# Kernel optimization log

Hardware: AMD Instinct MI355X
Metric: run time of the kernel (lower is better)

The kernel has to match this reference:

```python
import jax, jax.numpy as jnp
import numpy as np

B = 2048      # batch
C = 200       # n_country
F = 32        # n_feat_country == n_input
H = 256       # n_hidden


def setup_inputs() -> dict:
    key = jax.random.key(0)
    ks = jax.random.split(key, 9)
    x = jax.random.normal(ks[0], (B, C * F), dtype=jnp.float32)
    transition = jax.random.uniform(ks[1], (C, C), dtype=jnp.float32) / C
    W1 = jax.random.normal(ks[2], (F, H), dtype=jnp.float32) * (1.0 / np.sqrt(F))
    b1 = jax.random.normal(ks[3], (H,), dtype=jnp.float32) * 0.01
    W2 = jax.random.normal(ks[4], (H, H), dtype=jnp.float32) * (1.0 / np.sqrt(H))
    b2 = jax.random.normal(ks[5], (H,), dtype=jnp.float32) * 0.01
    W3 = jax.random.normal(ks[6], (H, 1), dtype=jnp.float32) * (1.0 / np.sqrt(H))
    b3 = jax.random.normal(ks[7], (1,), dtype=jnp.float32) * 0.01
    return {"x": x, "transition": transition, "W1": W1, "b1": b1,
            "W2": W2, "b2": b2, "W3": W3, "b3": b3}


def reference(x, transition, W1, b1, W2, b2, W3, b3):
    Bsz, N = x.shape
    Cn = transition.shape[0]
    Ff = N // Cn
    xc = x.reshape(Bsz, Cn, Ff)            # per-country feature blocks
    S = xc[..., 0]                          # [B, C] susceptible (feature 0)
    I = xc[..., 1]                          # [B, C] infected   (feature 1)
    # transition-weighted neighbor aggregation (the python loop == one GEMM)
    sinflow = S @ transition                # [B, C]
    iinflow = I @ transition                # [B, C]
    outflow = 1.0 - jnp.diag(transition)    # [C]
    # shared tiny MLP applied per country (vectorized over C)
    h = jax.nn.relu(jnp.einsum('bcf,fh->bch', xc, W1) + b1)
    h = jax.nn.relu(jnp.einsum('bch,hk->bck', h, W2) + b2)
    lamb = (jnp.einsum('bch,ho->bco', h, W3) + b3)[..., 0]  # [B, C]
    dS = -lamb * S + sinflow - outflow * S
    dI = lamb * S + iinflow - outflow * I
    # interleave: pred[:, 2i] = S_i + dS_i, pred[:, 2i+1] = I_i + dI_i
    pred = jnp.stack([S + dS, I + dI], axis=-1).reshape(Bsz, 2 * Cn)
    return pred
```

## Files before the change

kernel.cpp:

```cpp
#include <hip/hip_runtime.h>
#include <stdint.h>

#define M_ROWS 409600
#define B_CNT  2048
#define C_CNT  200
#define N_TILES (M_ROWS / 64)
#define GRID_MLP 512

typedef __attribute__((ext_vector_type(8))) short bf16x8;
typedef __attribute__((ext_vector_type(4))) float f32x4;

__device__ __forceinline__ ushort f2bf(float f) {
    uint32_t u = __float_as_uint(f);
    u += 0x7fffu + ((u >> 16) & 1u);
    return (ushort)(u >> 16);
}

__device__ __forceinline__ uint32_t cvtpk_bf16(float lo, float hi) {
    uint32_t r;
    asm("v_cvt_pk_bf16_f32 %0, %1, %2" : "=v"(r) : "v"(lo), "v"(hi));
    return r;
}

__device__ __forceinline__ f32x4 mfma16(bf16x8 a, bf16x8 b, f32x4 c) {
    return __builtin_amdgcn_mfma_f32_16x16x32_bf16(a, b, c, 0, 0, 0);
}

__device__ __forceinline__ bf16x8 pack8(float4 a, float4 b) {
    bf16x8 r;
    r[0] = (short)f2bf(a.x); r[1] = (short)f2bf(a.y);
    r[2] = (short)f2bf(a.z); r[3] = (short)f2bf(a.w);
    r[4] = (short)f2bf(b.x); r[5] = (short)f2bf(b.y);
    r[6] = (short)f2bf(b.z); r[7] = (short)f2bf(b.w);
    return r;
}

__global__ __launch_bounds__(256) void prep_kernel(
    const float* __restrict__ x, const float* __restrict__ T,
    const float* __restrict__ W1, const float* __restrict__ W2,
    ushort* __restrict__ xb16, float* __restrict__ Sc, float* __restrict__ Ic,
    float* __restrict__ sinW, float* __restrict__ iinW,
    ushort* __restrict__ W1t, ushort* __restrict__ W2t, int do_xb) {
    int blk = blockIdx.x, t = threadIdx.x;
    if (blk < B_CNT) {
        __shared__ float Sr[C_CNT], Ir[C_CNT];
        const float4* xr = (const float4*)(x + (size_t)blk * 6400);
        ushort4* xw = (ushort4*)(xb16 + (size_t)blk * 6400);
#pragma unroll
        for (int i = 0; i < 7; ++i) {
            int i4 = i * 256 + t;
            if (i4 < 1600) {
                float4 v = xr[i4];
                if (do_xb) {
                    ushort4 u;
                    u.x = f2bf(v.x); u.y = f2bf(v.y);
                    u.z = f2bf(v.z); u.w = f2bf(v.w);
                    xw[i4] = u;
                }
                if ((i4 & 7) == 0) {
                    int c = i4 >> 3;
                    Sr[c] = v.x; Ir[c] = v.y;
                    Sc[blk * C_CNT + c] = v.x;
                    Ic[blk * C_CNT + c] = v.y;
                }
            }
        }
        __syncthreads();
        if (t < C_CNT) {
            float as = 0.f, ai = 0.f;
            for (int cp = 0; cp < C_CNT; ++cp) {
                float tv = T[cp * C_CNT + t];
                as = fmaf(Sr[cp], tv, as);
                ai = fmaf(Ir[cp], tv, ai);
            }
            sinW[blk * C_CNT + t] = as;
            iinW[blk * C_CNT + t] = ai;
        }
    } else if (blk < B_CNT + 256) {
        int n = blk - B_CNT;
        W2t[n * 256 + t] = f2bf(W2[t * 256 + n]);
    } else {
        int idx = (blk - B_CNT - 256) * 256 + t;
        int n = idx >> 5, k = idx & 31;
        W1t[idx] = f2bf(W1[k * 256 + n]);
    }
}

template <bool XB>
__global__ __launch_bounds__(256, 2) void mlp_kernel(
    const float* __restrict__ x,
    const ushort* __restrict__ xb16,
    const float* __restrict__ T,
    const float* __restrict__ b1,
    const float* __restrict__ b2,
    const float* __restrict__ W3,
    const float* __restrict__ b3,
    const ushort* __restrict__ W1t,
    const ushort* __restrict__ W2t,
    const float* __restrict__ Sc, const float* __restrict__ Ic,
    const float* __restrict__ sinW, const float* __restrict__ iinW,
    float* __restrict__ out) {
    constexpr int RS = 264;
    __shared__ ushort h1s[64 * RS];
    __shared__ float b1f[256], b2f[256], w3f[256];
    __shared__ float lamb2[2][4][64];

    const int tid  = threadIdx.x;
    const int w    = tid >> 6;
    const int lane = tid & 63;
    const int L    = lane & 15;
    const int q    = lane >> 4;

    b1f[tid] = b1[tid];
    b2f[tid] = b2[tid];
    w3f[tid] = W3[tid];
    const float b3v = b3[0];

    bf16x8 a2r[4][8];
#pragma unroll
    for (int i2 = 0; i2 < 4; ++i2)
#pragma unroll
        for (int kc = 0; kc < 8; ++kc)
            a2r[i2][kc] =
                *(const bf16x8*)(W2t + (64 * w + i2 * 16 + L) * 256 + kc * 32 + q * 8);

    bf16x8 aw[4];
#pragma unroll
    for (int i = 0; i < 4; ++i)
        aw[i] = *(const bf16x8*)(W1t + (64 * w + i * 16 + L) * 32 + q * 8);

    int tile = blockIdx.x;
    bf16x8 bx[4];
#pragma unroll
    for (int i = 0; i < 4; ++i) {
        if (XB) {
            bx[i] = *(const bf16x8*)(xb16 + (size_t)(tile * 64 + i * 16 + L) * 32 + q * 8);
        } else {
            const float4* xr =
                (const float4*)(x + (size_t)(tile * 64 + i * 16 + L) * 32 + q * 8);
            bx[i] = pack8(xr[0], xr[1]);
        }
    }

    float eS = 0.f, eI = 0.f, esv = 0.f, eiv = 0.f, eof = 0.f;
    int ptile = -1;
    int p = 0;

    for (; tile < N_TILES; tile += GRID_MLP) {
        f32x4 acc1[4][4];
#pragma unroll
        for (int i1 = 0; i1 < 4; ++i1)
#pragma unroll
            for (int im = 0; im < 4; ++im)
                acc1[i1][im] = mfma16(aw[i1], bx[im], (f32x4){0.f, 0.f, 0.f, 0.f});

        {
            int tn = tile + GRID_MLP;
            if (tn >= N_TILES) tn = tile;
            const size_t mn0 = (size_t)tn * 64;
#pragma unroll
            for (int i = 0; i < 4; ++i) {
                if (XB) {
                    bx[i] = *(const bf16x8*)(xb16 + (mn0 + i * 16 + L) * 32 + q * 8);
                } else {
                    const float4* xr =
                        (const float4*)(x + (mn0 + i * 16 + L) * 32 + q * 8);
                    bx[i] = pack8(xr[0], xr[1]);
                }
            }
        }

        __syncthreads();

#pragma unroll
        for (int i1 = 0; i1 < 4; ++i1) {
            int n1b = 64 * w + i1 * 16 + q * 4;
            const float4 bv = *reinterpret_cast<const float4*>(&b1f[n1b]);
#pragma unroll
            for (int im = 0; im < 4; ++im) {
                int m = im * 16 + L;
                float v0 = fmaxf(acc1[i1][im][0] + bv.x, 0.f);
                float v1 = fmaxf(acc1[i1][im][1] + bv.y, 0.f);
                float v2 = fmaxf(acc1[i1][im][2] + bv.z, 0.f);
                float v3 = fmaxf(acc1[i1][im][3] + bv.w, 0.f);
                uint2 pk;
                pk.x = cvtpk_bf16(v0, v1);
                pk.y = cvtpk_bf16(v2, v3);
                *reinterpret_cast<uint2*>(&h1s[m * RS + n1b]) = pk;
            }
        }

        if (ptile >= 0 && tid < 64) {
            int gm = ptile * 64 + tid;
            float lam = lamb2[p ^ 1][0][tid] + lamb2[p ^ 1][1][tid] +
                        lamb2[p ^ 1][2][tid] + lamb2[p ^ 1][3][tid] + b3v;
            float dS = -lam * eS + esv - eof * eS;
            float dI =  lam * eS + eiv - eof * eI;
            float2 o; o.x = eS + dS; o.y = eI + dI;
            ((float2*)out)[gm] = o;
        }

        __syncthreads();

        f32x4 acc2[4][4];
#pragma unroll
        for (int i2 = 0; i2 < 4; ++i2)
#pragma unroll
            for (int im = 0; im < 4; ++im) acc2[i2][im] = (f32x4){0.f, 0.f, 0.f, 0.f};

#pragma unroll
        for (int kc = 0; kc < 8; ++kc) {
            bf16x8 bh[4];
#pragma unroll
            for (int im = 0; im < 4; ++im) {
                int m = im * 16 + L;
                bh[im] = *(const bf16x8*)(&h1s[m * RS + kc * 32 + q * 8]);
            }
#pragma unroll
            for (int i2 = 0; i2 < 4; ++i2)
#pragma unroll
                for (int im = 0; im < 4; ++im)
                    acc2[i2][im] = mfma16(a2r[i2][kc], bh[im], acc2[i2][im]);
        }

        if (tid < 64) {
            int gm = tile * 64 + tid;
            eS  = Sc[gm];  eI  = Ic[gm];
            esv = sinW[gm]; eiv = iinW[gm];
            int c = gm % C_CNT;
            eof = 1.0f - T[c * C_CNT + c];
        }

        float part[4] = {0.f, 0.f, 0.f, 0.f};
#pragma unroll
        for (int i2 = 0; i2 < 4; ++i2) {
            int n2b = 64 * w + i2 * 16 + q * 4;
            const float4 b2v = *reinterpret_cast<const float4*>(&b2f[n2b]);
            const float4 w3v = *reinterpret_cast<const float4*>(&w3f[n2b]);
#pragma unroll
            for (int im = 0; im < 4; ++im) {
                float h0 = fmaxf(acc2[i2][im][0] + b2v.x, 0.f);
                float h1 = fmaxf(acc2[i2][im][1] + b2v.y, 0.f);
                float h2 = fmaxf(acc2[i2][im][2] + b2v.z, 0.f);
                float h3 = fmaxf(acc2[i2][im][3] + b2v.w, 0.f);
                part[im] = fmaf(h0, w3v.x, part[im]);
                part[im] = fmaf(h1, w3v.y, part[im]);
                part[im] = fmaf(h2, w3v.z, part[im]);
                part[im] = fmaf(h3, w3v.w, part[im]);
            }
        }
#pragma unroll
        for (int im = 0; im < 4; ++im) {
            float pp = part[im];
            pp += __shfl_xor(pp, 16);
            pp += __shfl_xor(pp, 32);
            if (q == 0) lamb2[p][w][im * 16 + L] = pp;
        }

        ptile = tile;
        p ^= 1;
    }

    __syncthreads();
    if (ptile >= 0 && tid < 64) {
        int gm = ptile * 64 + tid;
        float lam = lamb2[p ^ 1][0][tid] + lamb2[p ^ 1][1][tid] +
                    lamb2[p ^ 1][2][tid] + lamb2[p ^ 1][3][tid] + b3v;
        float dS = -lam * eS + esv - eof * eS;
        float dI =  lam * eS + eiv - eof * eI;
        float2 o; o.x = eS + dS; o.y = eI + dI;
        ((float2*)out)[gm] = o;
    }
}

extern "C" void kernel_launch(void* const* d_in, const int* in_sizes, int n_in,
                              void* d_out, int out_size, void* d_ws, size_t ws_size,
                              hipStream_t stream) {
    const float* x  = (const float*)d_in[0];
    const float* T  = (const float*)d_in[1];
    const float* W1 = (const float*)d_in[2];
    const float* b1 = (const float*)d_in[3];
    const float* W2 = (const float*)d_in[4];
    const float* b2 = (const float*)d_in[5];
    const float* W3 = (const float*)d_in[6];
    const float* b3 = (const float*)d_in[7];

    const size_t xb_bytes = (size_t)M_ROWS * 32 * 2;
    const size_t f32_arr  = (size_t)M_ROWS * 4;
    const size_t small    = 4 * f32_arr + 8192 * 2 + 65536 * 2;
    const int    do_xb    = (ws_size >= xb_bytes + small) ? 1 : 0;

    char* ws = (char*)d_ws;
    ushort* xb16 = (ushort*)ws;
    char* base = ws + (do_xb ? xb_bytes : 0);
    float*  Sc   = (float*)(base);
    float*  Ic   = (float*)(base + f32_arr);
    float*  sinW = (float*)(base + 2 * f32_arr);
    float*  iinW = (float*)(base + 3 * f32_arr);
    ushort* W1t  = (ushort*)(base + 4 * f32_arr);
    ushort* W2t  = (ushort*)(base + 4 * f32_arr + 8192 * 2);

    hipLaunchKernelGGL(prep_kernel, dim3(B_CNT + 256 + 32), dim3(256), 0, stream,
                       x, T, W1, W2, xb16, Sc, Ic, sinW, iinW, W1t, W2t, do_xb);
    if (do_xb) {
        hipLaunchKernelGGL((mlp_kernel<true>), dim3(GRID_MLP), dim3(256), 0, stream,
                           x, xb16, T, b1, b2, W3, b3, W1t, W2t, Sc, Ic, sinW, iinW,
                           (float*)d_out);
    } else {
        hipLaunchKernelGGL((mlp_kernel<false>), dim3(GRID_MLP), dim3(256), 0, stream,
                           x, xb16, T, b1, b2, W3, b3, W1t, W2t, Sc, Ic, sinW, iinW,
                           (float*)d_out);
    }
}
```

Before: 202.0 us.

## Double-buffer h1 in LDS, precompute epilogue terms, reload W1 per tile

```diff
diff --git a/kernel.cpp b/kernel.cpp
--- a/kernel.cpp
+++ b/kernel.cpp
@@ -38,8 +38,7 @@
 __global__ __launch_bounds__(256) void prep_kernel(
     const float* __restrict__ x, const float* __restrict__ T,
     const float* __restrict__ W1, const float* __restrict__ W2,
-    ushort* __restrict__ xb16, float* __restrict__ Sc, float* __restrict__ Ic,
-    float* __restrict__ sinW, float* __restrict__ iinW,
+    ushort* __restrict__ xb16, float4* __restrict__ epi,
     ushort* __restrict__ W1t, ushort* __restrict__ W2t, int do_xb) {
     int blk = blockIdx.x, t = threadIdx.x;
     if (blk < B_CNT) {
@@ -60,8 +59,6 @@
                 if ((i4 & 7) == 0) {
                     int c = i4 >> 3;
                     Sr[c] = v.x; Ir[c] = v.y;
-                    Sc[blk * C_CNT + c] = v.x;
-                    Ic[blk * C_CNT + c] = v.y;
                 }
             }
         }
@@ -73,8 +70,14 @@
                 as = fmaf(Sr[cp], tv, as);
                 ai = fmaf(Ir[cp], tv, ai);
             }
-            sinW[blk * C_CNT + t] = as;
-            iinW[blk * C_CNT + t] = ai;
+            float S = Sr[t], I = Ir[t];
+            float of = 1.0f - T[t * C_CNT + t];
+            float4 e;
+            e.x = S;
+            e.y = S + as - of * S;
+            e.z = I + ai - of * I;
+            e.w = 0.f;
+            epi[(size_t)blk * C_CNT + t] = e;
         }
     } else if (blk < B_CNT + 256) {
         int n = blk - B_CNT;
@@ -90,18 +93,16 @@
 __global__ __launch_bounds__(256, 2) void mlp_kernel(
     const float* __restrict__ x,
     const ushort* __restrict__ xb16,
-    const float* __restrict__ T,
     const float* __restrict__ b1,
     const float* __restrict__ b2,
     const float* __restrict__ W3,
     const float* __restrict__ b3,
     const ushort* __restrict__ W1t,
     const ushort* __restrict__ W2t,
-    const float* __restrict__ Sc, const float* __restrict__ Ic,
-    const float* __restrict__ sinW, const float* __restrict__ iinW,
+    const float4* __restrict__ epi,
     float* __restrict__ out) {
     constexpr int RS = 264;
-    __shared__ ushort h1s[64 * RS];
+    __shared__ ushort h1s[2][64 * RS];
     __shared__ float b1f[256], b2f[256], w3f[256];
     __shared__ float lamb2[2][4][64];
 
@@ -124,10 +125,7 @@
             a2r[i2][kc] =
                 *(const bf16x8*)(W2t + (64 * w + i2 * 16 + L) * 256 + kc * 32 + q * 8);
 
-    bf16x8 aw[4];
-#pragma unroll
-    for (int i = 0; i < 4; ++i)
-        aw[i] = *(const bf16x8*)(W1t + (64 * w + i * 16 + L) * 32 + q * 8);
+    uint64_t w1a = (uint64_t)(W1t + (64 * w + L) * 32 + q * 8);
 
     int tile = blockIdx.x;
     bf16x8 bx[4];
@@ -142,11 +140,19 @@
         }
     }
 
-    float eS = 0.f, eI = 0.f, esv = 0.f, eiv = 0.f, eof = 0.f;
+    float eS = 0.f, eP = 0.f, eQ = 0.f;
     int ptile = -1;
-    int p = 0;
+    int buf = 0, wp = 0;
+
+    __syncthreads();
 
     for (; tile < N_TILES; tile += GRID_MLP) {
+        asm volatile("" : "+v"(w1a));
+        bf16x8 aw[4];
+#pragma unroll
+        for (int i = 0; i < 4; ++i)
+            aw[i] = *(const bf16x8*)(w1a + (size_t)i * 1024);
+
         f32x4 acc1[4][4];
 #pragma unroll
         for (int i1 = 0; i1 < 4; ++i1)
@@ -169,8 +175,6 @@
                 }
             }
         }
-
-        __syncthreads();
 
 #pragma unroll
         for (int i1 = 0; i1 < 4; ++i1) {
@@ -186,21 +190,21 @@
                 uint2 pk;
                 pk.x = cvtpk_bf16(v0, v1);
                 pk.y = cvtpk_bf16(v2, v3);
-                *reinterpret_cast<uint2*>(&h1s[m * RS + n1b]) = pk;
-            }
-        }
+                *reinterpret_cast<uint2*>(&h1s[buf][m * RS + n1b]) = pk;
+            }
+        }
+
+        __syncthreads();
 
         if (ptile >= 0 && tid < 64) {
             int gm = ptile * 64 + tid;
-            float lam = lamb2[p ^ 1][0][tid] + lamb2[p ^ 1][1][tid] +
-                        lamb2[p ^ 1][2][tid] + lamb2[p ^ 1][3][tid] + b3v;
-            float dS = -lam * eS + esv - eof * eS;
-            float dI =  lam * eS + eiv - eof * eI;
-            float2 o; o.x = eS + dS; o.y = eI + dI;
+            float lam = lamb2[wp ^ 1][0][tid] + lamb2[wp ^ 1][1][tid] +
+                        lamb2[wp ^ 1][2][tid] + lamb2[wp ^ 1][3][tid] + b3v;
+            float2 o;
+            o.x = eP - lam * eS;
+            o.y = eQ + lam * eS;
             ((float2*)out)[gm] = o;
         }
-
-        __syncthreads();
 
         f32x4 acc2[4][4];
 #pragma unroll
@@ -214,21 +218,13 @@
 #pragma unroll
             for (int im = 0; im < 4; ++im) {
                 int m = im * 16 + L;
-                bh[im] = *(const bf16x8*)(&h1s[m * RS + kc * 32 + q * 8]);
+                bh[im] = *(const bf16x8*)(&h1s[buf][m * RS + kc * 32 + q * 8]);
             }
 #pragma unroll
             for (int i2 = 0; i2 < 4; ++i2)
 #pragma unroll
                 for (int im = 0; im < 4; ++im)
                     acc2[i2][im] = mfma16(a2r[i2][kc], bh[im], acc2[i2][im]);
-        }
-
-        if (tid < 64) {
-            int gm = tile * 64 + tid;
-            eS  = Sc[gm];  eI  = Ic[gm];
-            esv = sinW[gm]; eiv = iinW[gm];
-            int c = gm % C_CNT;
-            eof = 1.0f - T[c * C_CNT + c];
         }
 
         float part[4] = {0.f, 0.f, 0.f, 0.f};
@@ -249,26 +245,33 @@
                 part[im] = fmaf(h3, w3v.w, part[im]);
             }
         }
+
+        if (tid < 64) {
+            float4 e = epi[(size_t)tile * 64 + tid];
+            eS = e.x; eP = e.y; eQ = e.z;
+        }
+
 #pragma unroll
         for (int im = 0; im < 4; ++im) {
             float pp = part[im];
             pp += __shfl_xor(pp, 16);
             pp += __shfl_xor(pp, 32);
-            if (q == 0) lamb2[p][w][im * 16 + L] = pp;
+            if (q == 0) lamb2[wp][w][im * 16 + L] = pp;
         }
 
         ptile = tile;
-        p ^= 1;
+        buf ^= 1;
+        wp ^= 1;
     }
 
     __syncthreads();
     if (ptile >= 0 && tid < 64) {
         int gm = ptile * 64 + tid;
-        float lam = lamb2[p ^ 1][0][tid] + lamb2[p ^ 1][1][tid] +
-                    lamb2[p ^ 1][2][tid] + lamb2[p ^ 1][3][tid] + b3v;
-        float dS = -lam * eS + esv - eof * eS;
-        float dI =  lam * eS + eiv - eof * eI;
-        float2 o; o.x = eS + dS; o.y = eI + dI;
+        float lam = lamb2[wp ^ 1][0][tid] + lamb2[wp ^ 1][1][tid] +
+                    lamb2[wp ^ 1][2][tid] + lamb2[wp ^ 1][3][tid] + b3v;
+        float2 o;
+        o.x = eP - lam * eS;
+        o.y = eQ + lam * eS;
         ((float2*)out)[gm] = o;
     }
 }
@@ -286,29 +289,24 @@
     const float* b3 = (const float*)d_in[7];
 
     const size_t xb_bytes = (size_t)M_ROWS * 32 * 2;
-    const size_t f32_arr  = (size_t)M_ROWS * 4;
-    const size_t small    = 4 * f32_arr + 8192 * 2 + 65536 * 2;
+    const size_t epi_b    = (size_t)M_ROWS * 16;
+    const size_t small    = epi_b + 8192 * 2 + 65536 * 2;
     const int    do_xb    = (ws_size >= xb_bytes + small) ? 1 : 0;
 
     char* ws = (char*)d_ws;
     ushort* xb16 = (ushort*)ws;
     char* base = ws + (do_xb ? xb_bytes : 0);
-    float*  Sc   = (float*)(base);
-    float*  Ic   = (float*)(base + f32_arr);
-    float*  sinW = (float*)(base + 2 * f32_arr);
-    float*  iinW = (float*)(base + 3 * f32_arr);
-    ushort* W1t  = (ushort*)(base + 4 * f32_arr);
-    ushort* W2t  = (ushort*)(base + 4 * f32_arr + 8192 * 2);
+    float4* epi  = (float4*)(base);
+    ushort* W1t  = (ushort*)(base + epi_b);
+    ushort* W2t  = (ushort*)(base + epi_b + 8192 * 2);
 
     hipLaunchKernelGGL(prep_kernel, dim3(B_CNT + 256 + 32), dim3(256), 0, stream,
-                       x, T, W1, W2, xb16, Sc, Ic, sinW, iinW, W1t, W2t, do_xb);
+                       x, T, W1, W2, xb16, epi, W1t, W2t, do_xb);
     if (do_xb) {
         hipLaunchKernelGGL((mlp_kernel<true>), dim3(GRID_MLP), dim3(256), 0, stream,
-                           x, xb16, T, b1, b2, W3, b3, W1t, W2t, Sc, Ic, sinW, iinW,
-                           (float*)d_out);
+                           x, xb16, b1, b2, W3, b3, W1t, W2t, epi, (float*)d_out);
     } else {
         hipLaunchKernelGGL((mlp_kernel<false>), dim3(GRID_MLP), dim3(256), 0, stream,
-                           x, xb16, T, b1, b2, W3, b3, W1t, W2t, Sc, Ic, sinW, iinW,
-                           (float*)d_out);
-    }
-}
+                           x, xb16, b1, b2, W3, b3, W1t, W2t, epi, (float*)d_out);
+    }
+}
```

Result: faster. 182.8 us (-9.5%).
